# Performance work log

Hardware: AMD Instinct MI355X
Metric: run time of the kernel (lower is better)

## Reference

```python
import jax, jax.numpy as jnp
import numpy as np

N, F_IN, H, C, D, NH, L, FF = 4096, 256, 2, 64, 128, 4, 2, 2048
DEG = 32


def setup_inputs() -> dict:
    key = jax.random.key(0)
    ks = jax.random.split(key, 32)
    s = 0.05
    # graph: random edges + self loops (PyG GATConv adds self loops)
    src = jax.random.randint(ks[0], (N * DEG,), 0, N)
    dst = jax.random.randint(ks[1], (N * DEG,), 0, N)
    loop = jnp.arange(N)
    edge_index = jnp.stack([jnp.concatenate([src, loop]),
                            jnp.concatenate([dst, loop])]).astype(jnp.int64)
    inp = {
        'x': jax.random.normal(ks[2], (N, F_IN), jnp.float32),
        'edge_index': edge_index,
        'enc_w1': jax.random.normal(ks[3], (F_IN, 128), jnp.float32) * s,
        'enc_b1': jnp.zeros((128,), jnp.float32),
        'enc_w2': jax.random.normal(ks[4], (128, D), jnp.float32) * s,
        'enc_b2': jnp.zeros((D,), jnp.float32),
        'gat_w': jax.random.normal(ks[5], (D, H * C), jnp.float32) * s,
        'gat_asrc': jax.random.normal(ks[6], (H, C), jnp.float32) * s,
        'gat_adst': jax.random.normal(ks[7], (H, C), jnp.float32) * s,
        'gat_bias': jnp.zeros((H * C,), jnp.float32),
        't_wq': jax.random.normal(ks[8], (L, D, D), jnp.float32) * s,
        't_bq': jnp.zeros((L, D), jnp.float32),
        't_wk': jax.random.normal(ks[9], (L, D, D), jnp.float32) * s,
        't_bk': jnp.zeros((L, D), jnp.float32),
        't_wv': jax.random.normal(ks[10], (L, D, D), jnp.float32) * s,
        't_bv': jnp.zeros((L, D), jnp.float32),
        't_wo': jax.random.normal(ks[11], (L, D, D), jnp.float32) * s,
        't_bo': jnp.zeros((L, D), jnp.float32),
        't_ln1_g': jnp.ones((L, D), jnp.float32),
        't_ln1_b': jnp.zeros((L, D), jnp.float32),
        't_ln2_g': jnp.ones((L, D), jnp.float32),
        't_ln2_b': jnp.zeros((L, D), jnp.float32),
        't_w1': jax.random.normal(ks[12], (L, D, FF), jnp.float32) * s,
        't_b1': jnp.zeros((L, FF), jnp.float32),
        't_w2': jax.random.normal(ks[13], (L, FF, D), jnp.float32) * s,
        't_b2': jnp.zeros((L, D), jnp.float32),
    }
    return inp


def _layer_norm(v, g, b):
    m = v.mean(-1, keepdims=True)
    var = v.var(-1, keepdims=True)
    return (v - m) / jnp.sqrt(var + 1e-5) * g + b


def _forward(x, edge_index, enc_w1, enc_b1, enc_w2, enc_b2,
             gat_w, gat_asrc, gat_adst, gat_bias,
             t_wq, t_bq, t_wk, t_bk, t_wv, t_bv, t_wo, t_bo,
             t_ln1_g, t_ln1_b, t_ln2_g, t_ln2_b, t_w1, t_b1, t_w2, t_b2):
    n = x.shape[0]
    # encoder MLP: Linear -> ReLU -> Linear
    h = jnp.maximum(x @ enc_w1 + enc_b1, 0.0) @ enc_w2 + enc_b2  # [N, D]
    # GATConv (concat heads), dropout inactive (eval)
    heads, ch = gat_asrc.shape
    hh = (h @ gat_w).reshape(n, heads, ch)                       # [N, H, C]
    src, dst = edge_index[0], edge_index[1]
    a_src = (hh * gat_asrc).sum(-1)                              # [N, H]
    a_dst = (hh * gat_adst).sum(-1)
    e = jax.nn.leaky_relu(a_src[src] + a_dst[dst], 0.2)          # [E, H]
    # segment softmax over destination nodes
    e_max = jax.ops.segment_max(e, dst, num_segments=n)
    e_exp = jnp.exp(e - e_max[dst])
    denom = jax.ops.segment_sum(e_exp, dst, num_segments=n)
    alpha = e_exp / denom[dst]                                   # [E, H]
    agg = jax.ops.segment_sum(alpha[:, :, None] * hh[src], dst, num_segments=n)
    y = agg.reshape(n, heads * ch) + gat_bias                    # [N, D]
    # TransformerEncoder (post-LN, relu FFN), unbatched sequence of N nodes
    d = y.shape[-1]
    dh = d // NH
    for l in range(t_wq.shape[0]):
        q = (y @ t_wq[l] + t_bq[l]).reshape(n, NH, dh)
        k = (y @ t_wk[l] + t_bk[l]).reshape(n, NH, dh)
        v = (y @ t_wv[l] + t_bv[l]).reshape(n, NH, dh)
        scores = jnp.einsum('nhd,mhd->hnm', q, k) / jnp.sqrt(jnp.float32(dh))
        p = jax.nn.softmax(scores, axis=-1)
        a = jnp.einsum('hnm,mhd->nhd', p, v).reshape(n, d)
        a = a @ t_wo[l] + t_bo[l]
        y = _layer_norm(y + a, t_ln1_g[l], t_ln1_b[l])
        f = jnp.maximum(y @ t_w1[l] + t_b1[l], 0.0) @ t_w2[l] + t_b2[l]
        y = _layer_norm(y + f, t_ln2_g[l], t_ln2_b[l])
    return y


def reference(x, edge_index, enc_w1, enc_b1, enc_w2, enc_b2,
              gat_w, gat_asrc, gat_adst, gat_bias,
              t_wq, t_bq, t_wk, t_bk, t_wv, t_bv, t_wo, t_bo,
              t_ln1_g, t_ln1_b, t_ln2_g, t_ln2_b, t_w1, t_b1, t_w2, t_b2):
    return _forward(x, edge_index, enc_w1, enc_b1, enc_w2, enc_b2,
                    gat_w, gat_asrc, gat_adst, gat_bias,
                    t_wq, t_bq, t_wk, t_bk, t_wv, t_bv, t_wo, t_bo,
                    t_ln1_g, t_ln1_b, t_ln2_g, t_ln2_b, t_w1, t_b1, t_w2, t_b2)
```

## Files before the change

### kernel.cpp

```cpp
#include <hip/hip_runtime.h>

typedef unsigned short u16;
typedef unsigned int u32;
typedef __attribute__((ext_vector_type(8))) short bh8;
typedef __attribute__((ext_vector_type(4))) float fx4;
typedef __attribute__((ext_vector_type(4))) short s4;
typedef __attribute__((ext_vector_type(2))) unsigned int u32x2;

#define QS 0.2550437194342803f

__device__ __forceinline__ u16 f2bf(float f) {
    unsigned u = __float_as_uint(f);
    u += 0x7fffu + ((u >> 16) & 1u);
    return (u16)(u >> 16);
}

__device__ __forceinline__ u32 cvtpk(float lo, float hi) {
    u32 r;
    asm("v_cvt_pk_bf16_f32 %0, %1, %2" : "=v"(r) : "v"(lo), "v"(hi));
    return r;
}

__global__ __launch_bounds__(256) void prep_kernel(
    const float* x, const float* ew1, const float* ew2, const float* gw,
    const float* wq, const float* wk, const float* wv, const float* wo,
    const float* w1, const float* w2,
    const float* bq, const float* bk, const float* bv,
    u16* xb, u16* ew1t, u16* ew2t, u16* gwt,
    u16* wqkvt, float* bqkv, u16* wot, u16* w1t, u16* w2t)
{
    __shared__ u16 tile[64 * 65];
    int bid = blockIdx.x;
    const int t = threadIdx.x;

    if (bid < 128) {
        const float4* x4 = (const float4*)x;
        s4* o4 = (s4*)xb;
        #pragma unroll
        for (int i = 0; i < 8; i++) {
            int fi = bid * 2048 + i * 256 + t;
            float4 v = x4[fi];
            s4 o = { (short)f2bf(v.x), (short)f2bf(v.y), (short)f2bf(v.z), (short)f2bf(v.w) };
            o4[fi] = o;
        }
        return;
    }
    bid -= 128;
    if (bid < 1) {
        for (int idx = t; idx < 768; idx += 256) {
            int l = idx / 384, n = idx % 384;
            float v;
            if (n < 128)      v = bq[l * 128 + n] * QS;
            else if (n < 256) v = bk[l * 128 + n - 128];
            else              v = bv[l * 128 + n - 256];
            bqkv[idx] = v;
        }
        return;
    }
    bid -= 1;

    const float* src; u16* dst; int R, C, tr, tc; float sc = 1.f;
    if (bid < 8)            { src = ew1; dst = ew1t; R = 256; C = 128; tr = bid >> 1; tc = bid & 1; }
    else if ((bid -= 8) < 4)  { src = ew2; dst = ew2t; R = 128; C = 128; tr = bid >> 1; tc = bid & 1; }
    else if ((bid -= 4) < 4)  { src = gw;  dst = gwt;  R = 128; C = 128; tr = bid >> 1; tc = bid & 1; }
    else if ((bid -= 4) < 24) {
        int l = bid / 12, r2 = bid % 12, which = r2 >> 2, i = r2 & 3;
        R = 128; C = 128; tr = i >> 1; tc = i & 1;
        if (which == 0)      { src = wq + l * 16384; dst = wqkvt + l * 49152;         sc = QS; }
        else if (which == 1) { src = wk + l * 16384; dst = wqkvt + l * 49152 + 16384; }
        else                 { src = wv + l * 16384; dst = wqkvt + l * 49152 + 32768; }
    }
    else if ((bid -= 24) < 8)   { int l = bid >> 2, i = bid & 3;  src = wo + l * 16384; dst = wot + l * 16384; R = 128; C = 128; tr = i >> 1; tc = i & 1; }
    else if ((bid -= 8) < 128)  { int l = bid >> 6, i = bid & 63; src = w1 + (size_t)l * 262144; dst = w1t + (size_t)l * 262144; R = 128;  C = 2048; tr = i & 1;  tc = i >> 1; }
    else { bid -= 128;            int l = bid >> 6, i = bid & 63; src = w2 + (size_t)l * 262144; dst = w2t + (size_t)l * 262144; R = 2048; C = 128;  tr = i >> 1; tc = i & 1; }

    const int r = t >> 2, cs = (t & 3) * 16;
    const float* sp = src + (size_t)(tr * 64 + r) * C + tc * 64 + cs;
    #pragma unroll
    for (int j = 0; j < 16; j++) tile[r * 65 + cs + j] = f2bf(sp[j] * sc);
    __syncthreads();
    u16* dp = dst + (size_t)(tc * 64 + r) * R + tr * 64 + cs;
    #pragma unroll
    for (int j = 0; j < 16; j++) dp[j] = tile[(cs + j) * 65 + r];
}

__global__ __launch_bounds__(256) void gemm_bf16(
    const u16* __restrict__ A, const u16* __restrict__ Bt,
    const float* __restrict__ bias,
    float* __restrict__ Cf, u16* __restrict__ Cb, float* __restrict__ Cpart,
    u16* __restrict__ Cvt,
    int M, int N, int K, int relu, int kchunk, int ldc)
{
    __shared__ __align__(16) u16 As[2][64][40];
    __shared__ __align__(16) u16 Bs[2][64][40];
    const int m0 = blockIdx.x * 64, n0 = blockIdx.y * 64, z = blockIdx.z;
    const int tid = threadIdx.x;
    const int lane = tid & 63, w = tid >> 6;
    const int wm = (w >> 1) * 32, wn = (w & 1) * 32;
    const int l15 = lane & 15, l4 = lane >> 4;
    const int srow = tid >> 2, skq = (tid & 3) * 8;
    const int k0 = z * kchunk;

    const u16* Ap = A + (size_t)(m0 + srow) * K + k0 + skq;
    const u16* Bp = Bt + (size_t)(n0 + srow) * K + k0 + skq;

    fx4 acc00 = {0,0,0,0}, acc01 = {0,0,0,0}, acc10 = {0,0,0,0}, acc11 = {0,0,0,0};

    *(int4*)&As[0][srow][skq] = *(const int4*)Ap;
    *(int4*)&Bs[0][srow][skq] = *(const int4*)Bp;

    const int niter = kchunk >> 5;
    for (int it = 0; it < niter; it++) {
        const int cur = it & 1;
        int4 ar, br;
        __syncthreads();
        if (it + 1 < niter) {
            ar = *(const int4*)(Ap + (it + 1) * 32);
            br = *(const int4*)(Bp + (it + 1) * 32);
        }
        bh8 a0 = *(const bh8*)&As[cur][wm + l15][l4 * 8];
        bh8 a1 = *(const bh8*)&As[cur][wm + 16 + l15][l4 * 8];
        bh8 b0 = *(const bh8*)&Bs[cur][wn + l15][l4 * 8];
        bh8 b1 = *(const bh8*)&Bs[cur][wn + 16 + l15][l4 * 8];
        acc00 = __builtin_amdgcn_mfma_f32_16x16x32_bf16(a0, b0, acc00, 0, 0, 0);
        acc01 = __builtin_amdgcn_mfma_f32_16x16x32_bf16(a0, b1, acc01, 0, 0, 0);
        acc10 = __builtin_amdgcn_mfma_f32_16x16x32_bf16(a1, b0, acc10, 0, 0, 0);
        acc11 = __builtin_amdgcn_mfma_f32_16x16x32_bf16(a1, b1, acc11, 0, 0, 0);
        if (it + 1 < niter) {
            *(int4*)&As[cur ^ 1][srow][skq] = ar;
            *(int4*)&Bs[cur ^ 1][srow][skq] = br;
        }
    }

    fx4* accs[2][2] = {{&acc00, &acc01}, {&acc10, &acc11}};
    #pragma unroll
    for (int i = 0; i < 2; i++)
        #pragma unroll
        for (int j = 0; j < 2; j++) {
            int colg = n0 + wn + j * 16 + l15;
            int rowb = m0 + wm + i * 16 + l4 * 4;
            if (Cpart) {
                float* cp = Cpart + (size_t)z * M * N;
                #pragma unroll
                for (int r = 0; r < 4; r++)
                    cp[(size_t)(rowb + r) * N + colg] = (*accs[i][j])[r];
                continue;
            }
            float bvv = bias ? bias[colg] : 0.f;
            float vals[4];
            #pragma unroll
            for (int r = 0; r < 4; r++) {
                float v = (*accs[i][j])[r] + bvv;
                vals[r] = relu ? fmaxf(v, 0.f) : v;
            }
            if (Cvt && colg >= 256) {
                s4 pk = { (short)f2bf(vals[0]), (short)f2bf(vals[1]),
                          (short)f2bf(vals[2]), (short)f2bf(vals[3]) };
                *(s4*)&Cvt[(size_t)(colg - 256) * 4096 + rowb] = pk;
            } else {
                #pragma unroll
                for (int r = 0; r < 4; r++) {
                    if (Cf) Cf[(size_t)(rowb + r) * ldc + colg] = vals[r];
                    if (Cb) Cb[(size_t)(rowb + r) * ldc + colg] = f2bf(vals[r]);
                }
            }
        }
}

__global__ __launch_bounds__(256) void ffn_fused(
    const u16* __restrict__ A, const u16* __restrict__ W1t,
    const float* __restrict__ b1, const u16* __restrict__ W2t,
    float* __restrict__ part)
{
    __shared__ __align__(16) u16 Ab[64][136];
    __shared__ __align__(16) u16 Wb[64][136];
    __shared__ __align__(16) u16 Sb[64][72];
    const int m0 = blockIdx.x * 64, z = blockIdx.y;
    const int tid = threadIdx.x;
    const int lane = tid & 63, w = tid >> 6;
    const int wm = (w >> 1) * 32;
    const int wn = (w & 1) * 32;
    const int wn2 = (w & 1) * 64;
    const int l15 = lane & 15, l4 = lane >> 4;
    const int sr = tid >> 2, sc = (tid & 3) * 32;

    {
        const u16* ap = A + (size_t)(m0 + sr) * 128 + sc;
        #pragma unroll
        for (int i = 0; i < 4; i++)
            *(int4*)&Ab[sr][sc + i * 8] = *(const int4*)(ap + i * 8);
    }

    fx4 acc2[2][4] = {};

    for (int chunk = 0; chunk < 4; chunk++) {
        const int ffbase = z * 256 + chunk * 64;
        __syncthreads();
        {
            const u16* wp = W1t + (size_t)(ffbase + sr) * 128 + sc;
            #pragma unroll
            for (int i = 0; i < 4; i++)
                *(int4*)&Wb[sr][sc + i * 8] = *(const int4*)(wp + i * 8);
        }
        __syncthreads();

        fx4 s[2][2] = {};
        #pragma unroll
        for (int ks = 0; ks < 4; ks++) {
            bh8 af0 = *(const bh8*)&Ab[wm + l15][ks * 32 + l4 * 8];
            bh8 af1 = *(const bh8*)&Ab[wm + 16 + l15][ks * 32 + l4 * 8];
            bh8 bf0 = *(const bh8*)&Wb[wn + l15][ks * 32 + l4 * 8];
            bh8 bf1 = *(const bh8*)&Wb[wn + 16 + l15][ks * 32 + l4 * 8];
            s[0][0] = __builtin_amdgcn_mfma_f32_16x16x32_bf16(af0, bf0, s[0][0], 0, 0, 0);
            s[0][1] = __builtin_amdgcn_mfma_f32_16x16x32_bf16(af0, bf1, s[0][1], 0, 0, 0);
            s[1][0] = __builtin_amdgcn_mfma_f32_16x16x32_bf16(af1, bf0, s[1][0], 0, 0, 0);
            s[1][1] = __builtin_amdgcn_mfma_f32_16x16x32_bf16(af1, bf1, s[1][1], 0, 0, 0);
        }
        #pragma unroll
        for (int mi = 0; mi < 2; mi++)
            #pragma unroll
            for (int nj = 0; nj < 2; nj++) {
                float bv = b1[ffbase + wn + nj * 16 + l15];
                #pragma unroll
                for (int r = 0; r < 4; r++) {
                    float v = fmaxf(s[mi][nj][r] + bv, 0.f);
                    Sb[wm + mi * 16 + l4 * 4 + r][wn + nj * 16 + l15] = f2bf(v);
                }
            }
        __syncthreads();

        #pragma unroll
        for (int ks = 0; ks < 2; ks++) {
            bh8 af0 = *(const bh8*)&Sb[wm + l15][ks * 32 + l4 * 8];
            bh8 af1 = *(const bh8*)&Sb[wm + 16 + l15][ks * 32 + l4 * 8];
            #pragma unroll
            for (int nj = 0; nj < 4; nj++) {
                bh8 bf = *(const bh8*)&W2t[(size_t)(wn2 + nj * 16 + l15) * 2048 + ffbase + ks * 32 + l4 * 8];
                acc2[0][nj] = __builtin_amdgcn_mfma_f32_16x16x32_bf16(af0, bf, acc2[0][nj], 0, 0, 0);
                acc2[1][nj] = __builtin_amdgcn_mfma_f32_16x16x32_bf16(af1, bf, acc2[1][nj], 0, 0, 0);
            }
        }
    }

    float* cp = part + (size_t)z * 524288;
    #pragma unroll
    for (int mi = 0; mi < 2; mi++)
        #pragma unroll
        for (int nj = 0; nj < 4; nj++) {
            int colg = wn2 + nj * 16 + l15;
            int rowb = m0 + wm + mi * 16 + l4 * 4;
            #pragma unroll
            for (int r = 0; r < 4; r++)
                cp[(size_t)(rowb + r) * 128 + colg] = acc2[mi][nj][r];
        }
}

__global__ __launch_bounds__(128) void gat_prep(
    const float* __restrict__ hh, const float* __restrict__ asrc,
    const float* __restrict__ adst, float* __restrict__ an_src,
    float* __restrict__ an_dst, int* __restrict__ counts)
{
    int n = blockIdx.x, tid = threadIdx.x;
    if (tid == 0) counts[n] = 0;
    int head = tid >> 6, c = tid & 63;
    float v = hh[n * 128 + tid];
    float ps = v * asrc[head * 64 + c];
    float pd = v * adst[head * 64 + c];
    for (int off = 32; off; off >>= 1) { ps += __shfl_down(ps, off); pd += __shfl_down(pd, off); }
    if (c == 0) { an_src[n * 2 + head] = ps; an_dst[n * 2 + head] = pd; }
}

__global__ void count_edges(const int* __restrict__ dst, int* counts, int E) {
    int i = blockIdx.x * 256 + threadIdx.x;
    if (i < E) atomicAdd(&counts[dst[i]], 1);
}

__global__ __launch_bounds__(1024) void scan_kernel(const int* __restrict__ counts,
                                                    int* row_start, int* cursor) {
    __shared__ int wsum[16];
    int tid = threadIdx.x, lane = tid & 63, wv = tid >> 6;
    int b = tid * 4;
    int c0 = counts[b], c1 = counts[b+1], c2 = counts[b+2], c3 = counts[b+3];
    int sum = c0 + c1 + c2 + c3;
    int inc = sum;
    #pragma unroll
    for (int off = 1; off < 64; off <<= 1) {
        int v = __shfl_up(inc, off);
        if (lane >= off) inc += v;
    }
    if (lane == 63) wsum[wv] = inc;
    __syncthreads();
    int base = 0;
    #pragma unroll
    for (int i = 0; i < 16; i++) {
        int v = wsum[i];
        base += (i < wv) ? v : 0;
    }
    int excl = base + inc - sum;
    int r0 = excl, r1 = excl + c0, r2 = r1 + c1, r3 = r2 + c2;
    row_start[b] = r0; row_start[b+1] = r1; row_start[b+2] = r2; row_start[b+3] = r3;
    cursor[b] = r0; cursor[b+1] = r1; cursor[b+2] = r2; cursor[b+3] = r3;
    if (tid == 1023) row_start[4096] = base + inc;
}

__global__ void scatter_edges(const int* __restrict__ src, const int* __restrict__ dst,
                              int* cursor, int* csr_src, int E) {
    int i = blockIdx.x * 256 + threadIdx.x;
    if (i < E) { int pos = atomicAdd(&cursor[dst[i]], 1); csr_src[pos] = src[i]; }
}

__global__ __launch_bounds__(256) void gat_aggregate(
    const int* __restrict__ row_start, const int* __restrict__ csr_src,
    const float* __restrict__ an_src, const float* __restrict__ an_dst,
    const float* __restrict__ hh, const float* __restrict__ gbias,
    float* __restrict__ y32, u16* __restrict__ yb)
{
    int n = blockIdx.x, tid = threadIdx.x;
    const int lane = tid & 63, wv = tid >> 6;
    int start = row_start[n], end = row_start[n + 1];
    float ad0 = an_dst[n * 2 + 0], ad1 = an_dst[n * 2 + 1];
    __shared__ float rmx[4][2], rsm[4][2];
    __shared__ float sal0[128], sal1[128], sagg[256];
    __shared__ int sidx[128];

    float mx0 = -1e30f, mx1 = -1e30f;
    for (int i = start + tid; i < end; i += 256) {
        int s = csr_src[i];
        float e0 = an_src[s * 2 + 0] + ad0; e0 = e0 > 0.f ? e0 : 0.2f * e0;
        float e1 = an_src[s * 2 + 1] + ad1; e1 = e1 > 0.f ? e1 : 0.2f * e1;
        mx0 = fmaxf(mx0, e0); mx1 = fmaxf(mx1, e1);
    }
    for (int off = 32; off; off >>= 1) { mx0 = fmaxf(mx0, __shfl_down(mx0, off)); mx1 = fmaxf(mx1, __shfl_down(mx1, off)); }
    if (lane == 0) { rmx[wv][0] = mx0; rmx[wv][1] = mx1; }
    __syncthreads();
    mx0 = fmaxf(fmaxf(rmx[0][0], rmx[1][0]), fmaxf(rmx[2][0], rmx[3][0]));
    mx1 = fmaxf(fmaxf(rmx[0][1], rmx[1][1]), fmaxf(rmx[2][1], rmx[3][1]));

    float den0 = 0.f, den1 = 0.f;
    for (int i = start + tid; i < end; i += 256) {
        int s = csr_src[i];
        float e0 = an_src[s * 2 + 0] + ad0; e0 = e0 > 0.f ? e0 : 0.2f * e0;
        float e1 = an_src[s * 2 + 1] + ad1; e1 = e1 > 0.f ? e1 : 0.2f * e1;
        den0 += __expf(e0 - mx0); den1 += __expf(e1 - mx1);
    }
    for (int off = 32; off; off >>= 1) { den0 += __shfl_down(den0, off); den1 += __shfl_down(den1, off); }
    if (lane == 0) { rsm[wv][0] = den0; rsm[wv][1] = den1; }
    __syncthreads();
    den0 = rsm[0][0] + rsm[1][0] + rsm[2][0] + rsm[3][0];
    den1 = rsm[0][1] + rsm[1][1] + rsm[2][1] + rsm[3][1];
    float rd0 = 1.f / den0, rd1 = 1.f / den1;

    const int grp = tid >> 7, ch = tid & 127, head = ch >> 6;
    float agg = 0.f;
    for (int c0 = start; c0 < end; c0 += 128) {
        int cnt = min(128, end - c0);
        __syncthreads();
        if (tid < cnt) {
            int s = csr_src[c0 + tid];
            float e0 = an_src[s * 2 + 0] + ad0; e0 = e0 > 0.f ? e0 : 0.2f * e0;
            float e1 = an_src[s * 2 + 1] + ad1; e1 = e1 > 0.f ? e1 : 0.2f * e1;
            sal0[tid] = __expf(e0 - mx0) * rd0;
            sal1[tid] = __expf(e1 - mx1) * rd1;
            sidx[tid] = s;
        }
        __syncthreads();
        const float* sal = head ? sal1 : sal0;
        for (int j = grp; j < cnt; j += 2)
            agg += sal[j] * hh[(size_t)sidx[j] * 128 + ch];
    }
    sagg[tid] = agg;
    __syncthreads();
    if (tid < 128) {
        float v = sagg[tid] + sagg[tid + 128] + gbias[tid];
        y32[(size_t)n * 128 + tid] = v;
        yb[(size_t)n * 128 + tid] = f2bf(v);
    }
}

__global__ __launch_bounds__(256) void flash_attn_part(
    const u16* __restrict__ q, const u16* __restrict__ k,
    const u16* __restrict__ vt, float* __restrict__ po,
    float* __restrict__ pm, float* __restrict__ pl)
{
    __shared__ __align__(16) u16 Kb[2][64][40];
    __shared__ __align__(16) u16 Vb[2][32][72];
    __shared__ __align__(16) u16 Ps[4][16][72];
    const int q0 = blockIdx.x * 64, h = blockIdx.y, ch = blockIdx.z;
    const int tid = threadIdx.x;
    const int w = tid >> 6, lane = tid & 63, l15 = lane & 15, l4 = lane >> 4;

    bh8 qf = *(const bh8*)&q[(size_t)(q0 + w * 16 + l15) * 256 + h * 32 + l4 * 8];

    const int skey = tid >> 2, sds = (tid & 3) * 8;
    const int svd = tid >> 3, svk = (tid & 7) * 8;
    const u16* kgp = &k[(size_t)(ch * 1024 + skey) * 256 + h * 32 + sds];
    const u16* vgp = &vt[(size_t)(h * 32 + svd) * 4096 + ch * 1024 + svk];

    fx4 o0 = {0,0,0,0}, o1 = {0,0,0,0};
    float M = -1e30f, L = 0.f;

    *(int4*)&Kb[0][skey][sds] = *(const int4*)kgp;
    *(int4*)&Vb[0][svd][svk] = *(const int4*)vgp;

    for (int ti = 0; ti < 16; ti++) {
        const int cur = ti & 1;
        int4 kr, vr;
        __syncthreads();
        if (ti < 15) {
            kr = *(const int4*)(kgp + (size_t)(ti + 1) * 64 * 256);
            vr = *(const int4*)(vgp + (ti + 1) * 64);
        }

        fx4 s[4];
        #pragma unroll
        for (int sub = 0; sub < 4; sub++) {
            bh8 kf = *(const bh8*)&Kb[cur][sub * 16 + l15][l4 * 8];
            fx4 z = {0,0,0,0};
            s[sub] = __builtin_amdgcn_mfma_f32_16x16x32_bf16(kf, qf, z, 0, 0, 0);
        }
        float t0 = fmaxf(fmaxf(s[0][0], s[0][1]), s[0][2]);
        float t1 = fmaxf(fmaxf(s[0][3], s[1][0]), s[1][1]);
        float t2 = fmaxf(fmaxf(s[1][2], s[1][3]), s[2][0]);
        float t3 = fmaxf(fmaxf(s[2][1], s[2][2]), s[2][3]);
        float t4 = fmaxf(fmaxf(s[3][0], s[3][1]), s[3][2]);
        float pmax = fmaxf(fmaxf(fmaxf(t0, t1), t2), fmaxf(fmaxf(t3, t4), s[3][3]));
        pmax = fmaxf(pmax, __shfl_xor(pmax, 16));
        pmax = fmaxf(pmax, __shfl_xor(pmax, 32));
        if (!__all(pmax - M <= 8.0f)) {
            float f = __builtin_amdgcn_exp2f(M - pmax);
            M = pmax;
            o0 *= f; o1 *= f; L *= f;
        }

        #pragma unroll
        for (int sub = 0; sub < 4; sub++)
            #pragma unroll
            for (int r = 0; r < 4; r++)
                s[sub][r] = __builtin_amdgcn_exp2f(s[sub][r] - M);
        float ss0 = (s[0][0] + s[0][1]) + (s[0][2] + s[0][3]);
        float ss1 = (s[1][0] + s[1][1]) + (s[1][2] + s[1][3]);
        float ss2 = (s[2][0] + s[2][1]) + (s[2][2] + s[2][3]);
        float ss3 = (s[3][0] + s[3][1]) + (s[3][2] + s[3][3]);
        float lsum = (ss0 + ss1) + (ss2 + ss3);
        lsum += __shfl_xor(lsum, 16);
        lsum += __shfl_xor(lsum, 32);
        L += lsum;

        #pragma unroll
        for (int sub = 0; sub < 4; sub++) {
            u32x2 pk = { cvtpk(s[sub][0], s[sub][1]), cvtpk(s[sub][2], s[sub][3]) };
            *(u32x2*)&Ps[w][l15][sub * 16 + l4 * 4] = pk;
        }

        #pragma unroll
        for (int kc = 0; kc < 2; kc++) {
            bh8 bf  = *(const bh8*)&Ps[w][l15][kc * 32 + l4 * 8];
            bh8 af0 = *(const bh8*)&Vb[cur][l15][kc * 32 + l4 * 8];
            bh8 af1 = *(const bh8*)&Vb[cur][16 + l15][kc * 32 + l4 * 8];
            o0 = __builtin_amdgcn_mfma_f32_16x16x32_bf16(af0, bf, o0, 0, 0, 0);
            o1 = __builtin_amdgcn_mfma_f32_16x16x32_bf16(af1, bf, o1, 0, 0, 0);
        }

        if (ti < 15) {
            *(int4*)&Kb[cur ^ 1][skey][sds] = kr;
            *(int4*)&Vb[cur ^ 1][svd][svk] = vr;
        }
    }
    const int base = (blockIdx.x * 4 + h) * 4 + ch;
    const int qrow = w * 16 + l15;
    *(fx4*)&po[(size_t)(base * 64 + qrow) * 32 + l4 * 4]      = o0;
    *(fx4*)&po[(size_t)(base * 64 + qrow) * 32 + 16 + l4 * 4] = o1;
    if (l4 == 0) { pm[base * 64 + qrow] = M; pl[base * 64 + qrow] = L; }
}

__global__ __launch_bounds__(256) void attn_combine(
    const float* __restrict__ po, const float* __restrict__ pm,
    const float* __restrict__ pl, u16* __restrict__ out)
{
    int qb = blockIdx.x, h = blockIdx.y;
    int col = threadIdx.x & 31, r0 = threadIdx.x >> 5;
    int rb = (qb * 4 + h) * 4;
    for (int j = 0; j < 8; j++) {
        int row = r0 * 8 + j;
        float m = -1e30f;
        for (int c = 0; c < 4; c++) m = fmaxf(m, pm[(rb + c) * 64 + row]);
        float l = 0.f, o = 0.f;
        for (int c = 0; c < 4; c++) {
            float wgt = __builtin_amdgcn_exp2f(pm[(rb + c) * 64 + row] - m);
            l += wgt * pl[(rb + c) * 64 + row];
            o += wgt * po[(size_t)((rb + c) * 64 + row) * 32 + col];
        }
        out[(size_t)(qb * 64 + row) * 128 + h * 32 + col] = f2bf(o / l);
    }
}

__global__ __launch_bounds__(256) void oproj_ln(
    const u16* __restrict__ A, const u16* __restrict__ Bt,
    const float* __restrict__ bias, const float* __restrict__ g,
    const float* __restrict__ b,
    float* __restrict__ y32, u16* __restrict__ yb)
{
    __shared__ __align__(16) u16 As[2][32][40];
    __shared__ __align__(16) u16 Bs[2][128][40];
    __shared__ float Ct[32][132];
    const int m0 = blockIdx.x * 32;
    const int tid = threadIdx.x;
    const int lane = tid & 63, w = tid >> 6;
    const int wm = (w >> 1) * 16, wn = (w & 1) * 64;
    const int l15 = lane & 15, l4 = lane >> 4;

    const int arow = tid >> 2, akq = (tid & 3) * 8;
    const u16* Ap  = A + (size_t)(m0 + arow) * 128 + akq;
    const u16* Bp0 = Bt + (size_t)arow * 128 + akq;
    const u16* Bp1 = Bp0 + (size_t)64 * 128;

    fx4 acc[4] = {};

    if (tid < 128) *(int4*)&As[0][arow][akq] = *(const int4*)Ap;
    *(int4*)&Bs[0][arow][akq]      = *(const int4*)Bp0;
    *(int4*)&Bs[0][arow + 64][akq] = *(const int4*)Bp1;

    for (int it = 0; it < 4; it++) {
        const int cur = it & 1;
        int4 ar, br0, br1;
        __syncthreads();
        if (it < 3) {
            if (tid < 128) ar = *(const int4*)(Ap + (it + 1) * 32);
            br0 = *(const int4*)(Bp0 + (it + 1) * 32);
            br1 = *(const int4*)(Bp1 + (it + 1) * 32);
        }
        bh8 af = *(const bh8*)&As[cur][wm + l15][l4 * 8];
        #pragma unroll
        for (int nj = 0; nj < 4; nj++) {
            bh8 bf = *(const bh8*)&Bs[cur][wn + nj * 16 + l15][l4 * 8];
            acc[nj] = __builtin_amdgcn_mfma_f32_16x16x32_bf16(af, bf, acc[nj], 0, 0, 0);
        }
        if (it < 3) {
            if (tid < 128) *(int4*)&As[cur ^ 1][arow][akq] = ar;
            *(int4*)&Bs[cur ^ 1][arow][akq]      = br0;
            *(int4*)&Bs[cur ^ 1][arow + 64][akq] = br1;
        }
    }

    #pragma unroll
    for (int nj = 0; nj < 4; nj++) {
        int cl = wn + nj * 16 + l15;
        float bvv = bias[cl];
        #pragma unroll
        for (int r = 0; r < 4; r++) {
            int rl = wm + l4 * 4 + r;
            Ct[rl][cl] = acc[nj][r] + bvv + y32[(size_t)(m0 + rl) * 128 + cl];
        }
    }
    __syncthreads();

    const int row = tid >> 3, c0 = (tid & 7) * 16;
    float s1 = 0.f, s2 = 0.f;
    #pragma unroll
    for (int j = 0; j < 16; j++) { float v = Ct[row][c0 + j]; s1 += v; s2 += v * v; }
    #pragma unroll
    for (int off = 1; off < 8; off <<= 1) { s1 += __shfl_xor(s1, off); s2 += __shfl_xor(s2, off); }
    float mean = s1 * (1.f / 128.f);
    float var = s2 * (1.f / 128.f) - mean * mean;
    float rstd = rsqrtf(var + 1e-5f);
    #pragma unroll
    for (int j = 0; j < 16; j++) {
        int col = c0 + j;
        float o = (Ct[row][col] - mean) * rstd * g[col] + b[col];
        y32[(size_t)(m0 + row) * 128 + col] = o;
        yb[(size_t)(m0 + row) * 128 + col] = f2bf(o);
    }
}

__global__ __launch_bounds__(128) void add_ln_p(
    const float* __restrict__ y, const float* __restrict__ part, int nz,
    const float* __restrict__ bias,
    const float* __restrict__ g, const float* __restrict__ b,
    float* __restrict__ out32, u16* __restrict__ outb)
{
    int n = blockIdx.x, tid = threadIdx.x;
    float v = y[(size_t)n * 128 + tid] + bias[tid];
    for (int z = 0; z < nz; z++) v += part[(size_t)z * 524288 + n * 128 + tid];
    float sacc = v;
    for (int off = 32; off; off >>= 1) sacc += __shfl_down(sacc, off);
    __shared__ float sm[2], sv[2];
    if ((tid & 63) == 0) sm[tid >> 6] = sacc;
    __syncthreads();
    float mean = (sm[0] + sm[1]) * (1.f / 128.f);
    float d = v - mean;
    float qacc = d * d;
    for (int off = 32; off; off >>= 1) qacc += __shfl_down(qacc, off);
    if ((tid & 63) == 0) sv[tid >> 6] = qacc;
    __syncthreads();
    float var = (sv[0] + sv[1]) * (1.f / 128.f);
    float o = d * rsqrtf(var + 1e-5f) * g[tid] + b[tid];
    out32[(size_t)n * 128 + tid] = o;
    outb[(size_t)n * 128 + tid] = f2bf(o);
}

extern "C" void kernel_launch(void* const* d_in, const int* in_sizes, int n_in,
                              void* d_out, int out_size, void* d_ws, size_t ws_size,
                              hipStream_t stream)
{
    const float* x     = (const float*)d_in[0];
    const int*   ei    = (const int*)  d_in[1];
    const float* ew1   = (const float*)d_in[2];
    const float* eb1   = (const float*)d_in[3];
    const float* ew2   = (const float*)d_in[4];
    const float* eb2   = (const float*)d_in[5];
    const float* gw    = (const float*)d_in[6];
    const float* gasrc = (const float*)d_in[7];
    const float* gadst = (const float*)d_in[8];
    const float* gbias = (const float*)d_in[9];
    const float* wq    = (const float*)d_in[10];
    const float* bq    = (const float*)d_in[11];
    const float* wk    = (const float*)d_in[12];
    const float* bk    = (const float*)d_in[13];
    const float* wv    = (const float*)d_in[14];
    const float* bv    = (const float*)d_in[15];
    const float* wo    = (const float*)d_in[16];
    const float* bo    = (const float*)d_in[17];
    const float* ln1g  = (const float*)d_in[18];
    const float* ln1b  = (const float*)d_in[19];
    const float* ln2g  = (const float*)d_in[20];
    const float* ln2b  = (const float*)d_in[21];
    const float* w1    = (const float*)d_in[22];
    const float* b1    = (const float*)d_in[23];
    const float* w2    = (const float*)d_in[24];
    const float* b2    = (const float*)d_in[25];

    const int E = in_sizes[1] / 2;
    const int* esrc = ei;
    const int* edst = ei + E;

    char* p = (char*)d_ws;
    auto alloc = [&](size_t bytes) -> void* {
        void* r = (void*)p;
        p += (bytes + 255) & ~(size_t)255;
        return r;
    };
    u16* xb    = (u16*)alloc(4096 * 256 * 2);
    u16* ew1t  = (u16*)alloc(128 * 256 * 2);
    u16* ew2t  = (u16*)alloc(128 * 128 * 2);
    u16* gwt   = (u16*)alloc(128 * 128 * 2);
    u16* wqkvt = (u16*)alloc(2 * 384 * 128 * 2);
    float* bqkv = (float*)alloc(2 * 384 * 4);
    u16* wot   = (u16*)alloc(2 * 128 * 128 * 2);
    u16* w1t   = (u16*)alloc(2 * 2048 * 128 * 2);
    u16* w2t   = (u16*)alloc(2 * 128 * 2048 * 2);
    u16* h1b   = (u16*)alloc(4096 * 128 * 2);
    u16* hb    = (u16*)alloc(4096 * 128 * 2);
    float* hh  = (float*)alloc(4096 * 128 * 4);
    float* ansrc = (float*)alloc(4096 * 2 * 4);
    float* andst = (float*)alloc(4096 * 2 * 4);
    int* counts    = (int*)alloc(4096 * 4);
    int* row_start = (int*)alloc(4097 * 4);
    int* cursor    = (int*)alloc(4096 * 4);
    int* csr_src   = (int*)alloc((size_t)E * 4);
    float* y32 = (float*)alloc(4096 * 128 * 4);
    u16* yb    = (u16*)alloc(4096 * 128 * 2);
    u16* qkvb  = (u16*)alloc((size_t)4096 * 256 * 2);
    u16* vtb   = (u16*)alloc(4096 * 128 * 2);
    u16* attnb = (u16*)alloc(4096 * 128 * 2);
    float* po  = (float*)alloc((size_t)64 * 4 * 4 * 64 * 32 * 4);
    float* pm  = (float*)alloc(64 * 4 * 4 * 64 * 4);
    float* pl  = (float*)alloc(64 * 4 * 4 * 64 * 4);
    float* ffpart = (float*)alloc((size_t)8 * 4096 * 128 * 4);

    prep_kernel<<<433, 256, 0, stream>>>(x, ew1, ew2, gw, wq, wk, wv, wo, w1, w2,
                                         bq, bk, bv,
                                         xb, ew1t, ew2t, gwt, wqkvt, bqkv, wot, w1t, w2t);

    gemm_bf16<<<dim3(64, 2), 256, 0, stream>>>(xb, ew1t, eb1, nullptr, h1b, nullptr, nullptr, 4096, 128, 256, 1, 256, 128);
    gemm_bf16<<<dim3(64, 2), 256, 0, stream>>>(h1b, ew2t, eb2, nullptr, hb, nullptr, nullptr, 4096, 128, 128, 0, 128, 128);

    gemm_bf16<<<dim3(64, 2), 256, 0, stream>>>(hb, gwt, nullptr, hh, nullptr, nullptr, nullptr, 4096, 128, 128, 0, 128, 128);
    gat_prep<<<4096, 128, 0, stream>>>(hh, gasrc, gadst, ansrc, andst, counts);
    count_edges<<<(E + 255) / 256, 256, 0, stream>>>(edst, counts, E);
    scan_kernel<<<1, 1024, 0, stream>>>(counts, row_start, cursor);
    scatter_edges<<<(E + 255) / 256, 256, 0, stream>>>(esrc, edst, cursor, csr_src, E);
    gat_aggregate<<<4096, 256, 0, stream>>>(row_start, csr_src, ansrc, andst, hh, gbias, y32, yb);

    for (int l = 0; l < 2; l++) {
        gemm_bf16<<<dim3(64, 6), 256, 0, stream>>>(yb, wqkvt + l * 49152, bqkv + l * 384, nullptr, qkvb, nullptr, vtb, 4096, 384, 128, 0, 128, 256);
        flash_attn_part<<<dim3(64, 4, 4), 256, 0, stream>>>(qkvb, qkvb + 128, vtb, po, pm, pl);
        attn_combine<<<dim3(64, 4), 256, 0, stream>>>(po, pm, pl, attnb);
        oproj_ln<<<128, 256, 0, stream>>>(attnb, wot + l * 16384, bo + l * 128, ln1g + l * 128, ln1b + l * 128, y32, yb);
        ffn_fused<<<dim3(64, 8), 256, 0, stream>>>(yb, w1t + (size_t)l * 262144, b1 + l * 2048, w2t + (size_t)l * 262144, ffpart);
        float* outp = (l == 1) ? (float*)d_out : y32;
        add_ln_p<<<4096, 128, 0, stream>>>(y32, ffpart, 8, b2 + l * 128, ln2g + l * 128, ln2b + l * 128, outp, yb);
    }
}
```

Measured before the change: 195.4 us.

## Fuse encoder-2, GAT linear and attention-logit prep; fold attention combine into o-proj LN

The second encoder GEMM, the GAT linear GEMM and the per-node attention-logit reduction are merged into one kernel that keeps the intermediate tile in shared memory. The split-K flash-attention combine step moves into the output-projection + LayerNorm kernel, which builds its bf16 A tile directly from the partial outputs. This drops several launches and the global round-trips for the hb and attnb buffers. In exchange it adds per-block staging work and larger shared-memory use, and runs the fused GAT stage on only 128 blocks.

Result: faster. 184.0 us, median of 2 (-5.8%).

```diff
diff --git a/kernel.cpp b/kernel.cpp
--- a/kernel.cpp
+++ b/kernel.cpp
@@ -167,6 +167,139 @@
         }
 }
 
+__global__ __launch_bounds__(256) void enc2_gat(
+    const u16* __restrict__ h1b, const u16* __restrict__ ew2t,
+    const float* __restrict__ eb2, const u16* __restrict__ gwt,
+    const float* __restrict__ gasrc, const float* __restrict__ gadst,
+    float* __restrict__ hh, float* __restrict__ ansrc,
+    float* __restrict__ andst, int* __restrict__ counts)
+{
+    __shared__ __align__(16) u16 As[32][136];
+    __shared__ __align__(16) u16 Bs[2][128][40];
+    __shared__ __align__(16) u16 Hb[32][136];
+    __shared__ float Ct[32][132];
+    const int m0 = blockIdx.x * 32;
+    const int tid = threadIdx.x;
+    const int lane = tid & 63, w = tid >> 6;
+    const int wm = (w >> 1) * 16, wn = (w & 1) * 64;
+    const int l15 = lane & 15, l4 = lane >> 4;
+
+    if (tid < 32) counts[blockIdx.x * 32 + tid] = 0;
+
+    {
+        const int row = tid >> 3, c0 = (tid & 7) * 16;
+        const u16* ap = h1b + (size_t)(m0 + row) * 128 + c0;
+        *(int4*)&As[row][c0]     = *(const int4*)ap;
+        *(int4*)&As[row][c0 + 8] = *(const int4*)(ap + 8);
+    }
+    {
+        #pragma unroll
+        for (int i = 0; i < 2; i++) {
+            int s = tid + i * 256, r = s >> 2, c = (s & 3) * 8;
+            *(int4*)&Bs[0][r][c] = *(const int4*)&ew2t[(size_t)r * 128 + c];
+        }
+    }
+
+    fx4 acc[4] = {};
+    for (int it = 0; it < 4; it++) {
+        const int cur = it & 1;
+        int4 br[2];
+        __syncthreads();
+        if (it < 3) {
+            #pragma unroll
+            for (int i = 0; i < 2; i++) {
+                int s = tid + i * 256, r = s >> 2, c = (s & 3) * 8;
+                br[i] = *(const int4*)&ew2t[(size_t)r * 128 + (it + 1) * 32 + c];
+            }
+        }
+        bh8 af = *(const bh8*)&As[wm + l15][it * 32 + l4 * 8];
+        #pragma unroll
+        for (int nj = 0; nj < 4; nj++) {
+            bh8 bf = *(const bh8*)&Bs[cur][wn + nj * 16 + l15][l4 * 8];
+            acc[nj] = __builtin_amdgcn_mfma_f32_16x16x32_bf16(af, bf, acc[nj], 0, 0, 0);
+        }
+        if (it < 3) {
+            #pragma unroll
+            for (int i = 0; i < 2; i++) {
+                int s = tid + i * 256, r = s >> 2, c = (s & 3) * 8;
+                *(int4*)&Bs[cur ^ 1][r][c] = br[i];
+            }
+        }
+    }
+
+    #pragma unroll
+    for (int nj = 0; nj < 4; nj++) {
+        int cl = wn + nj * 16 + l15;
+        float bvv = eb2[cl];
+        #pragma unroll
+        for (int r = 0; r < 4; r++)
+            Hb[wm + l4 * 4 + r][cl] = f2bf(acc[nj][r] + bvv);
+    }
+    {
+        #pragma unroll
+        for (int i = 0; i < 2; i++) {
+            int s = tid + i * 256, r = s >> 2, c = (s & 3) * 8;
+            *(int4*)&Bs[0][r][c] = *(const int4*)&gwt[(size_t)r * 128 + c];
+        }
+    }
+
+    fx4 acc2[4] = {};
+    for (int it = 0; it < 4; it++) {
+        const int cur = it & 1;
+        int4 br[2];
+        __syncthreads();
+        if (it < 3) {
+            #pragma unroll
+            for (int i = 0; i < 2; i++) {
+                int s = tid + i * 256, r = s >> 2, c = (s & 3) * 8;
+                br[i] = *(const int4*)&gwt[(size_t)r * 128 + (it + 1) * 32 + c];
+            }
+        }
+        bh8 af = *(const bh8*)&Hb[wm + l15][it * 32 + l4 * 8];
+        #pragma unroll
+        for (int nj = 0; nj < 4; nj++) {
+            bh8 bf = *(const bh8*)&Bs[cur][wn + nj * 16 + l15][l4 * 8];
+            acc2[nj] = __builtin_amdgcn_mfma_f32_16x16x32_bf16(af, bf, acc2[nj], 0, 0, 0);
+        }
+        if (it < 3) {
+            #pragma unroll
+            for (int i = 0; i < 2; i++) {
+                int s = tid + i * 256, r = s >> 2, c = (s & 3) * 8;
+                *(int4*)&Bs[cur ^ 1][r][c] = br[i];
+            }
+        }
+    }
+
+    #pragma unroll
+    for (int nj = 0; nj < 4; nj++) {
+        int cl = wn + nj * 16 + l15;
+        #pragma unroll
+        for (int r = 0; r < 4; r++) {
+            int rl = wm + l4 * 4 + r;
+            float v = acc2[nj][r];
+            hh[(size_t)(m0 + rl) * 128 + cl] = v;
+            Ct[rl][cl] = v;
+        }
+    }
+    __syncthreads();
+
+    const int row = tid >> 3, c0 = (tid & 7) * 16, head = c0 >> 6;
+    float ps = 0.f, pd = 0.f;
+    #pragma unroll
+    for (int j = 0; j < 16; j++) {
+        float v = Ct[row][c0 + j];
+        int cc = (c0 + j) & 63;
+        ps += v * gasrc[head * 64 + cc];
+        pd += v * gadst[head * 64 + cc];
+    }
+    ps += __shfl_xor(ps, 1); pd += __shfl_xor(pd, 1);
+    ps += __shfl_xor(ps, 2); pd += __shfl_xor(pd, 2);
+    if ((tid & 3) == 0) {
+        ansrc[(m0 + row) * 2 + head] = ps;
+        andst[(m0 + row) * 2 + head] = pd;
+    }
+}
+
 __global__ __launch_bounds__(256) void ffn_fused(
     const u16* __restrict__ A, const u16* __restrict__ W1t,
     const float* __restrict__ b1, const u16* __restrict__ W2t,
@@ -255,21 +388,6 @@
         }
 }
 
-__global__ __launch_bounds__(128) void gat_prep(
-    const float* __restrict__ hh, const float* __restrict__ asrc,
-    const float* __restrict__ adst, float* __restrict__ an_src,
-    float* __restrict__ an_dst, int* __restrict__ counts)
-{
-    int n = blockIdx.x, tid = threadIdx.x;
-    if (tid == 0) counts[n] = 0;
-    int head = tid >> 6, c = tid & 63;
-    float v = hh[n * 128 + tid];
-    float ps = v * asrc[head * 64 + c];
-    float pd = v * adst[head * 64 + c];
-    for (int off = 32; off; off >>= 1) { ps += __shfl_down(ps, off); pd += __shfl_down(pd, off); }
-    if (c == 0) { an_src[n * 2 + head] = ps; an_dst[n * 2 + head] = pd; }
-}
-
 __global__ void count_edges(const int* __restrict__ dst, int* counts, int E) {
     int i = blockIdx.x * 256 + threadIdx.x;
     if (i < E) atomicAdd(&counts[dst[i]], 1);
@@ -473,34 +591,14 @@
     if (l4 == 0) { pm[base * 64 + qrow] = M; pl[base * 64 + qrow] = L; }
 }
 
-__global__ __launch_bounds__(256) void attn_combine(
+__global__ __launch_bounds__(256) void oproj_cln(
     const float* __restrict__ po, const float* __restrict__ pm,
-    const float* __restrict__ pl, u16* __restrict__ out)
-{
-    int qb = blockIdx.x, h = blockIdx.y;
-    int col = threadIdx.x & 31, r0 = threadIdx.x >> 5;
-    int rb = (qb * 4 + h) * 4;
-    for (int j = 0; j < 8; j++) {
-        int row = r0 * 8 + j;
-        float m = -1e30f;
-        for (int c = 0; c < 4; c++) m = fmaxf(m, pm[(rb + c) * 64 + row]);
-        float l = 0.f, o = 0.f;
-        for (int c = 0; c < 4; c++) {
-            float wgt = __builtin_amdgcn_exp2f(pm[(rb + c) * 64 + row] - m);
-            l += wgt * pl[(rb + c) * 64 + row];
-            o += wgt * po[(size_t)((rb + c) * 64 + row) * 32 + col];
-        }
-        out[(size_t)(qb * 64 + row) * 128 + h * 32 + col] = f2bf(o / l);
-    }
-}
-
-__global__ __launch_bounds__(256) void oproj_ln(
-    const u16* __restrict__ A, const u16* __restrict__ Bt,
+    const float* __restrict__ pl, const u16* __restrict__ Bt,
     const float* __restrict__ bias, const float* __restrict__ g,
     const float* __restrict__ b,
     float* __restrict__ y32, u16* __restrict__ yb)
 {
-    __shared__ __align__(16) u16 As[2][32][40];
+    __shared__ __align__(16) u16 Ab[32][136];
     __shared__ __align__(16) u16 Bs[2][128][40];
     __shared__ float Ct[32][132];
     const int m0 = blockIdx.x * 32;
@@ -509,36 +607,65 @@
     const int wm = (w >> 1) * 16, wn = (w & 1) * 64;
     const int l15 = lane & 15, l4 = lane >> 4;
 
-    const int arow = tid >> 2, akq = (tid & 3) * 8;
-    const u16* Ap  = A + (size_t)(m0 + arow) * 128 + akq;
-    const u16* Bp0 = Bt + (size_t)arow * 128 + akq;
-    const u16* Bp1 = Bp0 + (size_t)64 * 128;
+    {
+        const int row = tid >> 3, c0 = (tid & 7) * 16;
+        const int gr = m0 + row, qb = gr >> 6, r64 = gr & 63, h = c0 >> 5;
+        const int rb = (qb * 4 + h) * 4;
+        float mv0 = pm[(rb + 0) * 64 + r64], mv1 = pm[(rb + 1) * 64 + r64];
+        float mv2 = pm[(rb + 2) * 64 + r64], mv3 = pm[(rb + 3) * 64 + r64];
+        float ms = fmaxf(fmaxf(mv0, mv1), fmaxf(mv2, mv3));
+        float wc[4];
+        wc[0] = __builtin_amdgcn_exp2f(mv0 - ms);
+        wc[1] = __builtin_amdgcn_exp2f(mv1 - ms);
+        wc[2] = __builtin_amdgcn_exp2f(mv2 - ms);
+        wc[3] = __builtin_amdgcn_exp2f(mv3 - ms);
+        float lsum = wc[0] * pl[(rb + 0) * 64 + r64] + wc[1] * pl[(rb + 1) * 64 + r64]
+                   + wc[2] * pl[(rb + 2) * 64 + r64] + wc[3] * pl[(rb + 3) * 64 + r64];
+        float rl = 1.f / lsum;
+        const int cb = c0 & 31;
+        float o[16] = {};
+        #pragma unroll
+        for (int c = 0; c < 4; c++) {
+            const float* pp = po + ((size_t)((rb + c) * 64 + r64)) * 32 + cb;
+            #pragma unroll
+            for (int jj = 0; jj < 4; jj++) {
+                fx4 v = *(const fx4*)(pp + jj * 4);
+                o[jj * 4 + 0] += wc[c] * v[0];
+                o[jj * 4 + 1] += wc[c] * v[1];
+                o[jj * 4 + 2] += wc[c] * v[2];
+                o[jj * 4 + 3] += wc[c] * v[3];
+            }
+        }
+        #pragma unroll
+        for (int j = 0; j < 16; j++)
+            Ab[row][c0 + j] = f2bf(o[j] * rl);
+    }
+
+    {
+        const int brow = tid >> 2, bkq = (tid & 3) * 8;
+        *(int4*)&Bs[0][brow][bkq]      = *(const int4*)&Bt[(size_t)brow * 128 + bkq];
+        *(int4*)&Bs[0][brow + 64][bkq] = *(const int4*)&Bt[(size_t)(brow + 64) * 128 + bkq];
+    }
 
     fx4 acc[4] = {};
-
-    if (tid < 128) *(int4*)&As[0][arow][akq] = *(const int4*)Ap;
-    *(int4*)&Bs[0][arow][akq]      = *(const int4*)Bp0;
-    *(int4*)&Bs[0][arow + 64][akq] = *(const int4*)Bp1;
-
+    const int brow = tid >> 2, bkq = (tid & 3) * 8;
     for (int it = 0; it < 4; it++) {
         const int cur = it & 1;
-        int4 ar, br0, br1;
+        int4 br0, br1;
         __syncthreads();
         if (it < 3) {
-            if (tid < 128) ar = *(const int4*)(Ap + (it + 1) * 32);
-            br0 = *(const int4*)(Bp0 + (it + 1) * 32);
-            br1 = *(const int4*)(Bp1 + (it + 1) * 32);
-        }
-        bh8 af = *(const bh8*)&As[cur][wm + l15][l4 * 8];
+            br0 = *(const int4*)&Bt[(size_t)brow * 128 + (it + 1) * 32 + bkq];
+            br1 = *(const int4*)&Bt[(size_t)(brow + 64) * 128 + (it + 1) * 32 + bkq];
+        }
+        bh8 af = *(const bh8*)&Ab[wm + l15][it * 32 + l4 * 8];
         #pragma unroll
         for (int nj = 0; nj < 4; nj++) {
             bh8 bf = *(const bh8*)&Bs[cur][wn + nj * 16 + l15][l4 * 8];
             acc[nj] = __builtin_amdgcn_mfma_f32_16x16x32_bf16(af, bf, acc[nj], 0, 0, 0);
         }
         if (it < 3) {
-            if (tid < 128) *(int4*)&As[cur ^ 1][arow][akq] = ar;
-            *(int4*)&Bs[cur ^ 1][arow][akq]      = br0;
-            *(int4*)&Bs[cur ^ 1][arow + 64][akq] = br1;
+            *(int4*)&Bs[cur ^ 1][brow][bkq]      = br0;
+            *(int4*)&Bs[cur ^ 1][brow + 64][bkq] = br1;
         }
     }
 
@@ -649,7 +776,6 @@
     u16* w1t   = (u16*)alloc(2 * 2048 * 128 * 2);
     u16* w2t   = (u16*)alloc(2 * 128 * 2048 * 2);
     u16* h1b   = (u16*)alloc(4096 * 128 * 2);
-    u16* hb    = (u16*)alloc(4096 * 128 * 2);
     float* hh  = (float*)alloc(4096 * 128 * 4);
     float* ansrc = (float*)alloc(4096 * 2 * 4);
     float* andst = (float*)alloc(4096 * 2 * 4);
@@ -661,7 +787,6 @@
     u16* yb    = (u16*)alloc(4096 * 128 * 2);
     u16* qkvb  = (u16*)alloc((size_t)4096 * 256 * 2);
     u16* vtb   = (u16*)alloc(4096 * 128 * 2);
-    u16* attnb = (u16*)alloc(4096 * 128 * 2);
     float* po  = (float*)alloc((size_t)64 * 4 * 4 * 64 * 32 * 4);
     float* pm  = (float*)alloc(64 * 4 * 4 * 64 * 4);
     float* pl  = (float*)alloc(64 * 4 * 4 * 64 * 4);
@@ -672,10 +797,7 @@
                                          xb, ew1t, ew2t, gwt, wqkvt, bqkv, wot, w1t, w2t);
 
     gemm_bf16<<<dim3(64, 2), 256, 0, stream>>>(xb, ew1t, eb1, nullptr, h1b, nullptr, nullptr, 4096, 128, 256, 1, 256, 128);
-    gemm_bf16<<<dim3(64, 2), 256, 0, stream>>>(h1b, ew2t, eb2, nullptr, hb, nullptr, nullptr, 4096, 128, 128, 0, 128, 128);
-
-    gemm_bf16<<<dim3(64, 2), 256, 0, stream>>>(hb, gwt, nullptr, hh, nullptr, nullptr, nullptr, 4096, 128, 128, 0, 128, 128);
-    gat_prep<<<4096, 128, 0, stream>>>(hh, gasrc, gadst, ansrc, andst, counts);
+    enc2_gat<<<128, 256, 0, stream>>>(h1b, ew2t, eb2, gwt, gasrc, gadst, hh, ansrc, andst, counts);
     count_edges<<<(E + 255) / 256, 256, 0, stream>>>(edst, counts, E);
     scan_kernel<<<1, 1024, 0, stream>>>(counts, row_start, cursor);
     scatter_edges<<<(E + 255) / 256, 256, 0, stream>>>(esrc, edst, cursor, csr_src, E);
@@ -684,8 +806,7 @@
     for (int l = 0; l < 2; l++) {
         gemm_bf16<<<dim3(64, 6), 256, 0, stream>>>(yb, wqkvt + l * 49152, bqkv + l * 384, nullptr, qkvb, nullptr, vtb, 4096, 384, 128, 0, 128, 256);
         flash_attn_part<<<dim3(64, 4, 4), 256, 0, stream>>>(qkvb, qkvb + 128, vtb, po, pm, pl);
-        attn_combine<<<dim3(64, 4), 256, 0, stream>>>(po, pm, pl, attnb);
-        oproj_ln<<<128, 256, 0, stream>>>(attnb, wot + l * 16384, bo + l * 128, ln1g + l * 128, ln1b + l * 128, y32, yb);
+        oproj_cln<<<128, 256, 0, stream>>>(po, pm, pl, wot + l * 16384, bo + l * 128, ln1g + l * 128, ln1b + l * 128, y32, yb);
         ffn_fused<<<dim3(64, 8), 256, 0, stream>>>(yb, w1t + (size_t)l * 262144, b1 + l * 2048, w2t + (size_t)l * 262144, ffpart);
         float* outp = (l == 1) ? (float*)d_out : y32;
         add_ln_p<<<4096, 128, 0, stream>>>(y32, ffpart, 8, b2 + l * 128, ln2g + l * 128, ln2b + l * 128, outp, yb);
```
